# Performance work log

Hardware: AMD Instinct MI355X
Metric: run time of the kernel (lower is better)

## Reference

```python
import jax, jax.numpy as jnp
import numpy as np

K, D = 512, 64

def setup_inputs() -> dict:
    key = jax.random.key(0)
    k1, k2 = jax.random.split(key)
    z_e_x = jax.random.normal(k1, (64, D, 64, 64), dtype=jnp.float32)  # [B, D, H, W]
    # nn.Embedding weight init: uniform(-1/K, 1/K)
    emb = jax.random.uniform(k2, (K, D), dtype=jnp.float32, minval=-1.0 / K, maxval=1.0 / K)
    return {"z_e_x": z_e_x, "emb": emb}

def reference(z_e_x, emb):
    # Squared L2 distance expanded: ||z||^2 - 2 z.e + ||e||^2, avoiding the
    # [B, K, D, H, W] broadcast intermediate of the original torch code.
    z_sq = jnp.sum(z_e_x * z_e_x, axis=1)              # [B, H, W]
    e_sq = jnp.sum(emb * emb, axis=1)                  # [K]
    cross = jnp.einsum('bdhw,kd->bkhw', z_e_x, emb)    # [B, K, H, W]
    dists = z_sq[:, None] - 2.0 * cross + e_sq[None, :, None, None]
    latents = jnp.argmin(dists, axis=1)                # [B, H, W] int
    return latents
```

## Files before the change

### kernel.cpp

```cpp
#include <hip/hip_runtime.h>

#define KCODES 512
#define DDIM 64

typedef __attribute__((ext_vector_type(8))) short bf16x8;
typedef __attribute__((ext_vector_type(4))) float f32x4;

#define WS_IMG    0
#define WS_ESQB   131072
#define WS_ESQ    133120
#define WS_MAXE   135168
#define WS_NEEDED 135172

__device__ __forceinline__ unsigned umin_(unsigned a, unsigned b) { return a < b ? a : b; }
__device__ __forceinline__ unsigned umax_(unsigned a, unsigned b) { return a > b ? a : b; }

__device__ __forceinline__ void bf16_split(float v, unsigned short& hi, unsigned short& lo) {
    unsigned u = __float_as_uint(v);
    unsigned r = u + 0x7fffu + ((u >> 16) & 1u);
    hi = (unsigned short)(r >> 16);
    float hf = __uint_as_float(((unsigned)hi) << 16);
    float l = v - hf;
    unsigned u2 = __float_as_uint(l);
    unsigned r2 = u2 + 0x7fffu + ((u2 >> 16) & 1u);
    lo = (unsigned short)(r2 >> 16);
}

__device__ __forceinline__ float np_dist_strided(const float* __restrict__ zp,
                                                 const float* __restrict__ e, float esqk) {
    float zq = 0.f, cr = 0.f;
    #pragma unroll 8
    for (int d = 0; d < DDIM; ++d) {
        float zv = zp[(size_t)d * 4096];
        zq = __fadd_rn(zq, __fmul_rn(zv, zv));
        cr = __fadd_rn(cr, __fmul_rn(zv, e[d]));
    }
    return __fadd_rn(__fsub_rn(zq, __fmul_rn(2.0f, cr)), esqk);
}

__global__ __launch_bounds__(512) void vq_pre_kernel(const float* __restrict__ emb,
                                                     char* __restrict__ ws)
{
    __shared__ float wmax[8];
    const int k = threadIdx.x;
    const float* e = emb + k * DDIM;

    float r[8];
    #pragma unroll
    for (int j = 0; j < 8; ++j) r[j] = __fmul_rn(e[j], e[j]);
    #pragma unroll
    for (int i = 8; i < DDIM; i += 8)
        #pragma unroll
        for (int j = 0; j < 8; ++j)
            r[j] = __fadd_rn(r[j], __fmul_rn(e[i + j], e[i + j]));
    float esq = __fadd_rn(
        __fadd_rn(__fadd_rn(r[0], r[1]), __fadd_rn(r[2], r[3])),
        __fadd_rn(__fadd_rn(r[4], r[5]), __fadd_rn(r[6], r[7])));
    ((float*)(ws + WS_ESQ))[k]  = esq;
    ((float*)(ws + WS_ESQB))[k] = __fadd_rn(esq, 0.5f);

    const int pass = k >> 6, rr = k & 63;
    unsigned short* ehi = (unsigned short*)(ws + WS_IMG + pass * 16384);
    unsigned short* elo = (unsigned short*)(ws + WS_IMG + pass * 16384 + 8192);
    float me = 0.f;
    #pragma unroll
    for (int jidx = 0; jidx < 8; ++jidx) {
        bf16x8 hh, ll;
        #pragma unroll
        for (int j = 0; j < 8; ++j) {
            float v = e[jidx * 8 + j];
            me = fmaxf(me, fabsf(v));
            unsigned short h, l;
            bf16_split(v, h, l);
            hh[j] = (short)h; ll[j] = (short)l;
        }
        int off = rr * 64 + ((jidx ^ (rr & 7)) << 3);
        *(bf16x8*)&ehi[off] = hh;
        *(bf16x8*)&elo[off] = ll;
    }

    #pragma unroll
    for (int m = 1; m < 64; m <<= 1) me = fmaxf(me, __shfl_xor(me, m));
    if ((k & 63) == 0) wmax[k >> 6] = me;
    __syncthreads();
    if (k == 0) {
        float M = wmax[0];
        #pragma unroll
        for (int i = 1; i < 8; ++i) M = fmaxf(M, wmax[i]);
        *(float*)(ws + WS_MAXE) = M;
    }
}

__global__ __launch_bounds__(256) void vq_main_kernel(
    const float* __restrict__ z, const float* __restrict__ emb,
    const char* __restrict__ ws, int* __restrict__ out)
{
    __shared__ __align__(16) unsigned short buf[2][8192];
    __shared__ __align__(16) float esqb[KCODES];

    const int t    = threadIdx.x;
    const int lane = t & 63;
    const int w    = t >> 6;
    const int g    = lane >> 4;
    const int p16  = lane & 15;

    esqb[t]       = ((const float*)(ws + WS_ESQB))[t];
    esqb[t + 256] = ((const float*)(ws + WS_ESQB))[t + 256];
    const float maxe = *((const float*)(ws + WS_MAXE));

    const int P0  = blockIdx.x * 256;
    const int bb  = P0 >> 12;
    const int hwW = (P0 & 4095) + w * 64;
    const float* zbase = z + (size_t)bb * (DDIM * 4096);

    bf16x8 zh[4][2], zl[4][2];
    float  sab[4];
    #pragma unroll
    for (int s = 0; s < 4; ++s) {
        sab[s] = 0.f;
        #pragma unroll
        for (int c = 0; c < 2; ++c) {
            #pragma unroll
            for (int j = 0; j < 8; ++j) {
                int d = g * 8 + j + c * 32;
                float v = zbase[(size_t)d * 4096 + hwW + s * 16 + p16];
                sab[s] += fabsf(v);
                unsigned short h, l;
                bf16_split(v, h, l);
                zh[s][c][j] = (short)h;
                zl[s][c][j] = (short)l;
            }
        }
    }

    const float4* img = (const float4*)(ws + WS_IMG);
    float4 st0, st1, st2, st3;
#define ISSUE(P)  { int b_ = (P) * 1024 + t; st0 = img[b_]; st1 = img[b_ + 256]; \
                    st2 = img[b_ + 512]; st3 = img[b_ + 768]; }
#define WRITEB(BI){ float4* dst_ = (float4*)&buf[BI][0]; dst_[t] = st0; dst_[t + 256] = st1; \
                    dst_[t + 512] = st2; dst_[t + 768] = st3; }

    ISSUE(0);
    WRITEB(0);
    ISSUE(1);
    __syncthreads();

    unsigned m1[4], m2[4], m3[4];
    #pragma unroll
    for (int s = 0; s < 4; ++s) { m1[s] = m2[s] = m3[s] = 0xFFFFFFFFu; }

    const int jj0 = g ^ (p16 & 7);
    const int jj1 = (4 + g) ^ (p16 & 7);
    const int g4  = g * 4;

    for (int pp = 0; pp < 8; ++pp) {
        const unsigned short* ehi = &buf[pp & 1][0];
        const unsigned short* elo = &buf[pp & 1][4096];

        #pragma unroll
        for (int tt = 0; tt < 4; ++tt) {
            const int row = tt * 16 + p16;
            const int ib0 = row * 64 + (jj0 << 3);
            const int ib1 = row * 64 + (jj1 << 3);
            bf16x8 ah0 = *(const bf16x8*)&ehi[ib0];
            bf16x8 ah1 = *(const bf16x8*)&ehi[ib1];
            bf16x8 al0 = *(const bf16x8*)&elo[ib0];
            bf16x8 al1 = *(const bf16x8*)&elo[ib1];
            const int ct = pp * 64 + tt * 16;
            f32x4 eq = *(const f32x4*)&esqb[ct + g4];
            const unsigned c0 = (unsigned)(ct + g4);

            #pragma unroll
            for (int s = 0; s < 4; ++s) {
                f32x4 acc = {0.f, 0.f, 0.f, 0.f};
                acc = __builtin_amdgcn_mfma_f32_16x16x32_bf16(ah0, zh[s][0], acc, 0, 0, 0);
                acc = __builtin_amdgcn_mfma_f32_16x16x32_bf16(ah1, zh[s][1], acc, 0, 0, 0);
                acc = __builtin_amdgcn_mfma_f32_16x16x32_bf16(al0, zh[s][0], acc, 0, 0, 0);
                acc = __builtin_amdgcn_mfma_f32_16x16x32_bf16(al1, zh[s][1], acc, 0, 0, 0);
                acc = __builtin_amdgcn_mfma_f32_16x16x32_bf16(ah0, zl[s][0], acc, 0, 0, 0);
                acc = __builtin_amdgcn_mfma_f32_16x16x32_bf16(ah1, zl[s][1], acc, 0, 0, 0);
                #pragma unroll
                for (int rr = 0; rr < 4; ++rr) {
                    float sc = fmaf(-2.f, acc[rr], eq[rr]);
                    unsigned key = (__float_as_uint(sc) & 0xFFFFFE00u) | (c0 + (unsigned)rr);
                    unsigned big  = umax_(key, m1[s]);
                    m1[s]         = umin_(key, m1[s]);
                    unsigned big2 = umax_(big, m2[s]);
                    m2[s]         = umin_(big, m2[s]);
                    m3[s]         = umin_(big2, m3[s]);
                }
            }
        }

        if (pp < 7) {
            WRITEB((pp + 1) & 1);
            if (pp < 6) ISSUE(pp + 2);
        }
        __syncthreads();
    }

    #pragma unroll
    for (int s = 0; s < 4; ++s) {
        #pragma unroll
        for (int st2 = 0; st2 < 2; ++st2) {
            const int mk = 16 << st2;
            unsigned b1 = (unsigned)__shfl_xor((int)m1[s], mk);
            unsigned b2 = (unsigned)__shfl_xor((int)m2[s], mk);
            unsigned b3 = (unsigned)__shfl_xor((int)m3[s], mk);
            float osa = __shfl_xor(sab[s], mk);
            sab[s] += osa;
            unsigned M1 = umin_(m1[s], b1), x = umax_(m1[s], b1);
            unsigned c  = umin_(m2[s], b2), d = umax_(m2[s], b2);
            unsigned M2 = umin_(x, c),      e2 = umax_(x, c);
            unsigned M3 = umin_(umin_(e2, d), umin_(m3[s], b3));
            m1[s] = M1; m2[s] = M2; m3[s] = M3;
        }
    }

    unsigned K1 = (g == 0) ? m1[0] : (g == 1) ? m1[1] : (g == 2) ? m1[2] : m1[3];
    unsigned K2 = (g == 0) ? m2[0] : (g == 1) ? m2[1] : (g == 2) ? m2[2] : m2[3];
    unsigned K3 = (g == 0) ? m3[0] : (g == 1) ? m3[1] : (g == 2) ? m3[2] : m3[3];
    float    SA = (g == 0) ? sab[0] : (g == 1) ? sab[1] : (g == 2) ? sab[2] : sab[3];

    const float qs1 = __uint_as_float(K1 & 0xFFFFFE00u);
    const float qs2 = __uint_as_float(K2 & 0xFFFFFE00u);
    const float qs3 = __uint_as_float(K3 & 0xFFFFFE00u);
    const int   I1  = (int)(K1 & 511u);
    const int   I2  = (int)(K2 & 511u);

    const float MARG = 1.0e-4f + 3.0e-5f * (SA * maxe);
    const bool  f2 = (qs2 - qs1) < MARG;
    const bool  f3 = ((qs3 - qs1) < MARG) || (2.f * SA * maxe > 0.45f) || !(qs1 > 0.f);

    const float* zrow = zbase + hwW + lane;
    const float* esqr = (const float*)(ws + WS_ESQ);
    int idx = I1;

    if (f2 && !f3) {
        int a = min(I1, I2), b = max(I1, I2);
        float Da = np_dist_strided(zrow, emb + a * DDIM, esqr[a]);
        float Db = np_dist_strided(zrow, emb + b * DDIM, esqr[b]);
        idx = (Db < Da) ? b : a;
    }

    unsigned long long bal = __ballot(f3);
    while (bal) {
        int pix = __ffsll((long long)bal) - 1;
        bal &= bal - 1;
        const float* zf = zbase + hwW + pix;
        float bD = 3.0e38f; int bC = 0;
        #pragma unroll
        for (int j = 0; j < 8; ++j) {
            int c = j * 64 + lane;
            float D = np_dist_strided(zf, emb + c * DDIM, esqr[c]);
            if (D < bD) { bD = D; bC = c; }
        }
        #pragma unroll
        for (int mk = 1; mk < 64; mk <<= 1) {
            float oD = __shfl_xor(bD, mk);
            int   oC = __shfl_xor(bC, mk);
            if (oD < bD || (oD == bD && oC < bC)) { bD = oD; bC = oC; }
        }
        if (lane == pix) idx = bC;
    }

    out[P0 + w * 64 + lane] = idx;
#undef ISSUE
#undef WRITEB
}

__device__ __forceinline__ float fb_fast_score(const float4* __restrict__ e4,
                                               const float* zr, float esqk)
{
    float a0 = 0.f, a1 = 0.f, a2 = 0.f, a3 = 0.f;
    #pragma unroll
    for (int i = 0; i < DDIM / 4; ++i) {
        float4 v = e4[i];
        a0 = fmaf(zr[4*i+0], v.x, a0);
        a1 = fmaf(zr[4*i+1], v.y, a1);
        a2 = fmaf(zr[4*i+2], v.z, a2);
        a3 = fmaf(zr[4*i+3], v.w, a3);
    }
    return fmaf(-2.f, (a0 + a1) + (a2 + a3), esqk);
}

__device__ __forceinline__ float fb_np_dist(const float* __restrict__ e,
                                            const float* zr, float zsq, float esqk)
{
    float c = 0.f;
    #pragma unroll
    for (int d = 0; d < DDIM; ++d)
        c = __fadd_rn(c, __fmul_rn(zr[d], e[d]));
    return __fadd_rn(__fsub_rn(zsq, __fmul_rn(2.0f, c)), esqk);
}

__global__ __launch_bounds__(256) void vq_fallback_kernel(
    const float* __restrict__ z, const float* __restrict__ emb, int* __restrict__ out)
{
    __shared__ float esq[KCODES];
    const int t = threadIdx.x;
    for (int k = t; k < KCODES; k += 256) {
        const float* e = emb + k * DDIM;
        float r[8];
        #pragma unroll
        for (int j = 0; j < 8; ++j) r[j] = __fmul_rn(e[j], e[j]);
        #pragma unroll
        for (int i = 8; i < DDIM; i += 8)
            #pragma unroll
            for (int j = 0; j < 8; ++j)
                r[j] = __fadd_rn(r[j], __fmul_rn(e[i+j], e[i+j]));
        esq[k] = __fadd_rn(
            __fadd_rn(__fadd_rn(r[0], r[1]), __fadd_rn(r[2], r[3])),
            __fadd_rn(__fadd_rn(r[4], r[5]), __fadd_rn(r[6], r[7])));
    }
    __syncthreads();
    const int p  = blockIdx.x * 256 + t;
    const int b  = p >> 12;
    const int hw = p & 4095;
    const float* zp = z + (size_t)b * (DDIM * 4096) + hw;
    float zr[DDIM];
    #pragma unroll
    for (int d = 0; d < DDIM; ++d) zr[d] = zp[(size_t)d * 4096];
    float zsq = __fmul_rn(zr[0], zr[0]);
    #pragma unroll
    for (int d = 1; d < DDIM; ++d)
        zsq = __fadd_rn(zsq, __fmul_rn(zr[d], zr[d]));
    float m1 = 3.0e38f, m2 = 3.0e38f, m3 = 3.0e38f;
    int   i1 = 0, i2 = 0;
    for (int k = 0; k < KCODES; ++k) {
        const float s = fb_fast_score(reinterpret_cast<const float4*>(emb + k * DDIM), zr, esq[k]);
        const bool b1 = s < m1, b2 = s < m2, b3 = s < m3;
        const float nm3 = b2 ? m2 : (b3 ? s : m3);
        const float nm2 = b1 ? m1 : (b2 ? s : m2);
        const int   ni2 = b1 ? i1 : (b2 ? k : i2);
        const float nm1 = b1 ? s : m1;
        const int   ni1 = b1 ? k : i1;
        m3 = nm3; m2 = nm2; i2 = ni2; m1 = nm1; i1 = ni1;
    }
    int idx = i1;
    if (m2 - m1 < 6.0e-5f) {
        if (m3 - m1 >= 6.0e-5f) {
            const float D1 = fb_np_dist(emb + i1 * DDIM, zr, zsq, esq[i1]);
            const float D2 = fb_np_dist(emb + i2 * DDIM, zr, zsq, esq[i2]);
            const int   ka = (i1 < i2) ? i1 : i2;
            const int   kb = (i1 < i2) ? i2 : i1;
            const float Da = (i1 < i2) ? D1 : D2;
            const float Db = (i1 < i2) ? D2 : D1;
            idx = (Db < Da) ? kb : ka;
        } else {
            float bestD = 3.0e38f; int bi = 0; bool found = false;
            for (int k = 0; k < KCODES; ++k) {
                const float s = fb_fast_score(reinterpret_cast<const float4*>(emb + k * DDIM), zr, esq[k]);
                if (s < m1 + 6.0e-5f) {
                    const float Dk = fb_np_dist(emb + k * DDIM, zr, zsq, esq[k]);
                    if (!found || Dk < bestD) { bestD = Dk; bi = k; found = true; }
                }
            }
            idx = bi;
        }
    }
    out[p] = idx;
}

extern "C" void kernel_launch(void* const* d_in, const int* in_sizes, int n_in,
                              void* d_out, int out_size, void* d_ws, size_t ws_size,
                              hipStream_t stream)
{
    const float* z   = (const float*)d_in[0];
    const float* emb = (const float*)d_in[1];
    int* out = (int*)d_out;
    if (ws_size >= (size_t)WS_NEEDED) {
        hipLaunchKernelGGL(vq_pre_kernel, dim3(1), dim3(512), 0, stream, emb, (char*)d_ws);
        hipLaunchKernelGGL(vq_main_kernel, dim3(out_size / 256), dim3(256), 0, stream,
                           z, emb, (const char*)d_ws, out);
    } else {
        hipLaunchKernelGGL(vq_fallback_kernel, dim3(out_size / 256), dim3(256), 0, stream,
                           z, emb, out);
    }
}
```

Measured before the change: 147.1 us.

## Defer ambiguous-pixel exact rechecks to a compacted tail kernel

Instead of resolving near-tie pixels inline (which stalls whole wavefronts on divergent strided fp32 loops), the main kernel appends ambiguous pixels to global work lists via atomics, and a separate tail kernel processes them densely. It also tightens the f2 margin, moves the first embedding-image prefetch earlier and the next-buffer write before compute, and adds a launch-bounds occupancy hint. This adds an extra kernel launch, global atomics, and a tighter margin that may risk correctness near ties.

```diff
diff --git a/kernel.cpp b/kernel.cpp
--- a/kernel.cpp
+++ b/kernel.cpp
@@ -10,7 +10,14 @@
 #define WS_ESQB   131072
 #define WS_ESQ    133120
 #define WS_MAXE   135168
-#define WS_NEEDED 135172
+#define WS_CNTA   135172
+#define WS_CNTB   135176
+#define WS_LISTA  135184
+#define WS_LISTB  200720
+#define CAPA      8192u
+#define CAPB      2048u
+#define WS_NEED_FULL 208912
+#define WS_NEED_BASE 135184
 
 __device__ __forceinline__ unsigned umin_(unsigned a, unsigned b) { return a < b ? a : b; }
 __device__ __forceinline__ unsigned umax_(unsigned a, unsigned b) { return a > b ? a : b; }
@@ -45,6 +52,8 @@
     const int k = threadIdx.x;
     const float* e = emb + k * DDIM;
 
+    if (k == 0) { *(unsigned*)(ws + WS_CNTA) = 0u; *(unsigned*)(ws + WS_CNTB) = 0u; }
+
     float r[8];
     #pragma unroll
     for (int j = 0; j < 8; ++j) r[j] = __fmul_rn(e[j], e[j]);
@@ -91,9 +100,10 @@
     }
 }
 
-__global__ __launch_bounds__(256) void vq_main_kernel(
+__global__ __launch_bounds__(256, 4) void vq_main_kernel(
     const float* __restrict__ z, const float* __restrict__ emb,
-    const char* __restrict__ ws, int* __restrict__ out)
+    char* __restrict__ ws, int* __restrict__ out,
+    unsigned capA, unsigned capB)
 {
     __shared__ __align__(16) unsigned short buf[2][8192];
     __shared__ __align__(16) float esqb[KCODES];
@@ -112,6 +122,15 @@
     const int bb  = P0 >> 12;
     const int hwW = (P0 & 4095) + w * 64;
     const float* zbase = z + (size_t)bb * (DDIM * 4096);
+
+    const float4* img = (const float4*)(ws + WS_IMG);
+    float4 st0, st1, st2, st3;
+#define ISSUE(P)  { int b_ = (P) * 1024 + t; st0 = img[b_]; st1 = img[b_ + 256]; \
+                    st2 = img[b_ + 512]; st3 = img[b_ + 768]; }
+#define WRITEB(BI){ float4* dst_ = (float4*)&buf[BI][0]; dst_[t] = st0; dst_[t + 256] = st1; \
+                    dst_[t + 512] = st2; dst_[t + 768] = st3; }
+
+    ISSUE(0);
 
     bf16x8 zh[4][2], zl[4][2];
     float  sab[4];
@@ -133,14 +152,6 @@
         }
     }
 
-    const float4* img = (const float4*)(ws + WS_IMG);
-    float4 st0, st1, st2, st3;
-#define ISSUE(P)  { int b_ = (P) * 1024 + t; st0 = img[b_]; st1 = img[b_ + 256]; \
-                    st2 = img[b_ + 512]; st3 = img[b_ + 768]; }
-#define WRITEB(BI){ float4* dst_ = (float4*)&buf[BI][0]; dst_[t] = st0; dst_[t + 256] = st1; \
-                    dst_[t + 512] = st2; dst_[t + 768] = st3; }
-
-    ISSUE(0);
     WRITEB(0);
     ISSUE(1);
     __syncthreads();
@@ -154,6 +165,11 @@
     const int g4  = g * 4;
 
     for (int pp = 0; pp < 8; ++pp) {
+        if (pp < 7) {
+            WRITEB((pp + 1) & 1);
+            if (pp < 6) ISSUE(pp + 2);
+        }
+
         const unsigned short* ehi = &buf[pp & 1][0];
         const unsigned short* elo = &buf[pp & 1][4096];
 
@@ -191,11 +207,6 @@
                 }
             }
         }
-
-        if (pp < 7) {
-            WRITEB((pp + 1) & 1);
-            if (pp < 6) ISSUE(pp + 2);
-        }
         __syncthreads();
     }
 
@@ -228,31 +239,84 @@
     const int   I1  = (int)(K1 & 511u);
     const int   I2  = (int)(K2 & 511u);
 
-    const float MARG = 1.0e-4f + 3.0e-5f * (SA * maxe);
+    const float MARG = 6.0e-5f + 3.0e-5f * (SA * maxe);
     const bool  f2 = (qs2 - qs1) < MARG;
     const bool  f3 = ((qs3 - qs1) < MARG) || (2.f * SA * maxe > 0.45f) || !(qs1 > 0.f);
 
-    const float* zrow = zbase + hwW + lane;
+    const int pix = P0 + w * 64 + lane;
+    bool ovf = false;
+    if (f3) {
+        unsigned i = atomicAdd((unsigned*)(ws + WS_CNTB), 1u);
+        if (i < capB) ((unsigned*)(ws + WS_LISTB))[i] = (unsigned)pix; else ovf = true;
+    } else if (f2) {
+        unsigned i = atomicAdd((unsigned*)(ws + WS_CNTA), 1u);
+        if (i < capA) {
+            unsigned a = (unsigned)min(I1, I2), b = (unsigned)max(I1, I2);
+            uint2 rec; rec.x = (unsigned)pix; rec.y = (a << 9) | b;
+            ((uint2*)(ws + WS_LISTA))[i] = rec;
+        } else ovf = true;
+    }
+
+    int idx = I1;
+    unsigned long long bal = __ballot(ovf);
+    if (bal) {
+        const float* esqr = (const float*)(ws + WS_ESQ);
+        while (bal) {
+            int pl = __ffsll((long long)bal) - 1;
+            bal &= bal - 1;
+            const float* zf = zbase + hwW + pl;
+            float bD = 3.0e38f; int bC = 0;
+            #pragma unroll
+            for (int j = 0; j < 8; ++j) {
+                int c = j * 64 + lane;
+                float D = np_dist_strided(zf, emb + c * DDIM, esqr[c]);
+                if (D < bD) { bD = D; bC = c; }
+            }
+            #pragma unroll
+            for (int mk = 1; mk < 64; mk <<= 1) {
+                float oD = __shfl_xor(bD, mk);
+                int   oC = __shfl_xor(bC, mk);
+                if (oD < bD || (oD == bD && oC < bC)) { bD = oD; bC = oC; }
+            }
+            if (lane == pl) idx = bC;
+        }
+    }
+    out[pix] = idx;
+#undef ISSUE
+#undef WRITEB
+}
+
+__global__ __launch_bounds__(256) void vq_tail_kernel(
+    const float* __restrict__ z, const float* __restrict__ emb,
+    char* __restrict__ ws, int* __restrict__ out, unsigned capA, unsigned capB)
+{
+    const unsigned nA = umin_(*(const unsigned*)(ws + WS_CNTA), capA);
+    const unsigned nB = umin_(*(const unsigned*)(ws + WS_CNTB), capB);
     const float* esqr = (const float*)(ws + WS_ESQ);
-    int idx = I1;
-
-    if (f2 && !f3) {
-        int a = min(I1, I2), b = max(I1, I2);
-        float Da = np_dist_strided(zrow, emb + a * DDIM, esqr[a]);
-        float Db = np_dist_strided(zrow, emb + b * DDIM, esqr[b]);
-        idx = (Db < Da) ? b : a;
-    }
-
-    unsigned long long bal = __ballot(f3);
-    while (bal) {
-        int pix = __ffsll((long long)bal) - 1;
-        bal &= bal - 1;
-        const float* zf = zbase + hwW + pix;
+    const unsigned gid  = blockIdx.x * 256 + threadIdx.x;
+    const unsigned gsz  = gridDim.x * 256;
+
+    for (unsigned i = gid; i < nA; i += gsz) {
+        uint2 rec = ((const uint2*)(ws + WS_LISTA))[i];
+        const int pix = (int)rec.x;
+        const int a = (int)((rec.y >> 9) & 511u), b = (int)(rec.y & 511u);
+        const float* zp = z + (size_t)(pix >> 12) * (DDIM * 4096) + (pix & 4095);
+        float Da = np_dist_strided(zp, emb + a * DDIM, esqr[a]);
+        float Db = np_dist_strided(zp, emb + b * DDIM, esqr[b]);
+        out[pix] = (Db < Da) ? b : a;
+    }
+
+    const unsigned wid  = gid >> 6;
+    const unsigned nwav = gsz >> 6;
+    const int lane = threadIdx.x & 63;
+    for (unsigned j = wid; j < nB; j += nwav) {
+        const int pix = (int)((const unsigned*)(ws + WS_LISTB))[j];
+        const float* zp = z + (size_t)(pix >> 12) * (DDIM * 4096) + (pix & 4095);
         float bD = 3.0e38f; int bC = 0;
         #pragma unroll
-        for (int j = 0; j < 8; ++j) {
-            int c = j * 64 + lane;
-            float D = np_dist_strided(zf, emb + c * DDIM, esqr[c]);
+        for (int q = 0; q < 8; ++q) {
+            int c = q * 64 + lane;
+            float D = np_dist_strided(zp, emb + c * DDIM, esqr[c]);
             if (D < bD) { bD = D; bC = c; }
         }
         #pragma unroll
@@ -261,12 +325,8 @@
             int   oC = __shfl_xor(bC, mk);
             if (oD < bD || (oD == bD && oC < bC)) { bD = oD; bC = oC; }
         }
-        if (lane == pix) idx = bC;
-    }
-
-    out[P0 + w * 64 + lane] = idx;
-#undef ISSUE
-#undef WRITEB
+        if (lane == 0) out[pix] = bC;
+    }
 }
 
 __device__ __forceinline__ float fb_fast_score(const float4* __restrict__ e4,
@@ -369,10 +429,16 @@
     const float* z   = (const float*)d_in[0];
     const float* emb = (const float*)d_in[1];
     int* out = (int*)d_out;
-    if (ws_size >= (size_t)WS_NEEDED) {
+    if (ws_size >= (size_t)WS_NEED_FULL) {
         hipLaunchKernelGGL(vq_pre_kernel, dim3(1), dim3(512), 0, stream, emb, (char*)d_ws);
         hipLaunchKernelGGL(vq_main_kernel, dim3(out_size / 256), dim3(256), 0, stream,
-                           z, emb, (const char*)d_ws, out);
+                           z, emb, (char*)d_ws, out, CAPA, CAPB);
+        hipLaunchKernelGGL(vq_tail_kernel, dim3(64), dim3(256), 0, stream,
+                           z, emb, (char*)d_ws, out, CAPA, CAPB);
+    } else if (ws_size >= (size_t)WS_NEED_BASE) {
+        hipLaunchKernelGGL(vq_pre_kernel, dim3(1), dim3(512), 0, stream, emb, (char*)d_ws);
+        hipLaunchKernelGGL(vq_main_kernel, dim3(out_size / 256), dim3(256), 0, stream,
+                           z, emb, (char*)d_ws, out, 0u, 0u);
     } else {
         hipLaunchKernelGGL(vq_fallback_kernel, dim3(out_size / 256), dim3(256), 0, stream,
                            z, emb, out);
```

Result: slower. 218.3 us (+48.4%).
